# Performance work log

Measured on AMD Instinct MI355X. Metric: run time of the kernel, lower is better.

Reference implementation:

```python
import jax, jax.numpy as jnp
import numpy as np

EPS = 1e-5
HALT_THRESHOLD = 0.01
DILATIONS = (1, 2, 4)


def layer_norm(x, g, b):
    m = jnp.mean(x, axis=-1, keepdims=True)
    v = jnp.var(x, axis=-1, keepdims=True)
    return (x - m) * jax.lax.rsqrt(v + EPS) * g + b


def depthwise_conv(x, k, dilation):
    # x: [B,H,W,C], k: [kh,kw,1,C] (groups == C)
    pad = dilation * (k.shape[0] // 2)
    return jax.lax.conv_general_dilated(
        x, k, window_strides=(1, 1), padding=[(pad, pad), (pad, pad)],
        rhs_dilation=(dilation, dilation),
        dimension_numbers=('NHWC', 'HWIO', 'NHWC'),
        feature_group_count=x.shape[-1])


def setup_inputs() -> dict:
    key = jax.random.key(0)
    ks = jax.random.split(key, 12)
    B, H, W, C = 8, 96, 96, 64
    hid = 64
    P = C + len(DILATIONS) * C  # 256
    n = jax.random.normal
    return {
        'x': n(ks[0], (B, H, W, C), dtype=jnp.float32),
        'g1': jnp.ones((C,), jnp.float32), 'b1': jnp.zeros((C,), jnp.float32),
        'g2': jnp.ones((P,), jnp.float32), 'b2': jnp.zeros((P,), jnp.float32),
        'k1': 0.2 * n(ks[1], (3, 3, 1, C), dtype=jnp.float32),
        'k2': 0.2 * n(ks[2], (3, 3, 1, C), dtype=jnp.float32),
        'k3': 0.2 * n(ks[3], (3, 3, 1, C), dtype=jnp.float32),
        'Wu1': n(ks[4], (P, 2 * hid), dtype=jnp.float32) / np.sqrt(P),
        'bu1': jnp.zeros((2 * hid,), jnp.float32),
        'Wu2': n(ks[5], (2 * hid, hid), dtype=jnp.float32) / np.sqrt(2 * hid),
        'bu2': jnp.zeros((hid,), jnp.float32),
        'Wu3': n(ks[6], (hid, C), dtype=jnp.float32) / np.sqrt(hid),
        'bu3': jnp.zeros((C,), jnp.float32),
        'gh': jnp.ones((C,), jnp.float32), 'bh': jnp.zeros((C,), jnp.float32),
        'Wh1': n(ks[7], (C, hid), dtype=jnp.float32) / np.sqrt(C),
        'bh1': jnp.zeros((hid,), jnp.float32),
        'Wh2': n(ks[8], (hid, 1), dtype=jnp.float32) / np.sqrt(hid),
        'bh2': jnp.zeros((1,), jnp.float32),
        'max_steps': 8, 'min_steps': 1,
    }


def reference(x, g1, b1, g2, b2, k1, k2, k3, Wu1, bu1, Wu2, bu2, Wu3, bu3,
              gh, bh, Wh1, bh1, Wh2, bh2, max_steps, min_steps):
    gelu = lambda t: jax.nn.gelu(t, approximate=False)

    def forward_step(xs):
        # halt unit: LN -> Linear -> GELU -> Linear -> sigmoid
        h = gelu(layer_norm(xs, gh, bh) @ Wh1 + bh1)
        halt_probs = jax.nn.sigmoid(h @ Wh2 + bh2)[..., 0]  # [B,H,W]
        xn = layer_norm(xs, g1, b1)
        ps = [depthwise_conv(xn, k, d) for k, d in zip((k1, k2, k3), DILATIONS)]
        u = layer_norm(jnp.concatenate([xn] + ps, axis=-1), g2, b2)
        h1 = gelu(u @ Wu1 + bu1)
        h2 = gelu(h1 @ Wu2 + bu2)
        delta = h2 @ Wu3 + bu3
        return delta, halt_probs

    B, H, W, C = x.shape
    halted0 = jnp.zeros((B, H, W), jnp.bool_)
    acc0 = jnp.zeros((B, H, W), x.dtype)
    so0 = jnp.zeros_like(x)
    pc0 = jnp.zeros((B, H, W), x.dtype)

    def body(carry, step):
        xs, halted, acc, so, pc = carry
        delta, hp = forward_step(xs)
        active = ~halted
        af = active.astype(xs.dtype)
        xs = xs + delta * af[..., None]
        in_halt_phase = step >= (min_steps - 1)
        acc_n = acc + hp * af
        should_halt = (acc_n > 1.0 - HALT_THRESHOLD) & active
        halt_w = jnp.where(should_halt, 1.0 - (acc_n - hp), hp * af)
        so_n = so + xs * halt_w[..., None]
        halted_n = halted | should_halt
        acc = jnp.where(in_halt_phase, acc_n, acc)
        so = jnp.where(in_halt_phase, so_n, so)
        halted = jnp.where(in_halt_phase, halted_n, halted)
        pc = pc + jnp.where(in_halt_phase, af, jnp.ones_like(pc))
        return (xs, halted, acc, so, pc), None

    (xf, halted, acc, so, pc), _ = jax.lax.scan(
        body, (x, halted0, acc0, so0, pc0), jnp.arange(max_steps))
    # distribute remaining probability mass to cells that never halted
    remaining_w = (~halted).astype(x.dtype) * (1.0 - acc)
    so = so + xf * remaining_w[..., None]
    pc = pc / max_steps
    return so, halted, pc
```

## Files before the change

kernel.cpp:

```cpp
#include <hip/hip_runtime.h>
#include <hip/hip_bf16.h>

#define NPIX 73728
#define CH 64
#define HH 96
#define WW 96
#define PP 256

typedef __attribute__((ext_vector_type(8))) short short8;
typedef __attribute__((ext_vector_type(4))) float f32x4;

__device__ __forceinline__ float wsum64(float v) {
#pragma unroll
  for (int off = 32; off > 0; off >>= 1) v += __shfl_xor(v, off, 64);
  return v;
}
__device__ __forceinline__ float wsum16(float v) {
#pragma unroll
  for (int off = 1; off < 16; off <<= 1) v += __shfl_xor(v, off, 64);
  return v;
}
__device__ __forceinline__ float gelu_f(float x) {
  return 0.5f * x * (1.0f + erff(x * 0.70710678118654752f));
}
__device__ __forceinline__ float b2f(ushort u) {
  union { unsigned int i; float f; } c;
  c.i = ((unsigned int)u) << 16;
  return c.f;
}
__device__ __forceinline__ ushort f2b(float f) {
  union { float f; unsigned int i; } c;
  c.f = f;
  unsigned int r = c.i + 0x7fff + ((c.i >> 16) & 1);
  return (ushort)(r >> 16);
}

__global__ __launch_bounds__(256) void k_init(const float* __restrict__ x,
                                              float* __restrict__ xs,
                                              float* __restrict__ out,
                                              float* __restrict__ accb,
                                              float* __restrict__ xnf) {
  int i = blockIdx.x * 256 + threadIdx.x;
  if (i < NPIX * CH) xs[i] = x[i];
  if (i < NPIX * 66) out[i] = 0.0f;
  if (i < NPIX) { accb[i] = 0.0f; xnf[i] = 0.0f; }
}

__global__ __launch_bounds__(256) void k_wprep(const float* __restrict__ W,
                                               ushort* __restrict__ Wp, int K,
                                               int N) {
  int t = blockIdx.x * 256 + threadIdx.x;
  if (t >= K * N) return;
  int j = t & 7, l = (t >> 3) & 63, tile = t >> 9;
  int NT = N >> 4;
  int kt = tile / NT, nt = tile - kt * NT;
  int k = kt * 32 + ((l >> 4) & 3) * 8 + j;
  int n = nt * 16 + (l & 15);
  Wp[t] = f2b(W[k * N + n]);
}

__global__ __launch_bounds__(256) void k_ln_halt(
    const float* __restrict__ xs, ushort* __restrict__ xn, float* __restrict__ hp,
    const float* __restrict__ halted, float* __restrict__ xnf,
    const float* __restrict__ g1, const float* __restrict__ b1,
    const float* __restrict__ gh, const float* __restrict__ bh,
    const float* __restrict__ Wh1, const float* __restrict__ bh1,
    const float* __restrict__ Wh2, const float* __restrict__ bh2) {
  __shared__ float lnbuf[4][64];
  int wave = threadIdx.x >> 6, lane = threadIdx.x & 63;
  int pix = blockIdx.x * 4 + wave;
  float hf = halted[pix];
  if (hf != 0.0f && xnf[pix] != 0.0f) return;
  float x = xs[(size_t)pix * CH + lane];
  float mean = wsum64(x) * (1.0f / 64.0f);
  float d = x - mean;
  float var = wsum64(d * d) * (1.0f / 64.0f);
  float rstd = rsqrtf(var + 1e-5f);
  float nrm = d * rstd;
  xn[(size_t)pix * CH + lane] = f2b(nrm * g1[lane] + b1[lane]);
  lnbuf[wave][lane] = nrm * gh[lane] + bh[lane];
  float acc = bh1[lane];
#pragma unroll 8
  for (int i = 0; i < 64; ++i)
    acc = fmaf(lnbuf[wave][i], Wh1[i * 64 + lane], acc);
  acc = gelu_f(acc);
  float c = wsum64(acc * Wh2[lane]);
  if (lane == 0) {
    hp[pix] = 1.0f / (1.0f + expf(-(c + bh2[0])));
    xnf[pix] = hf;
  }
}

template <bool EDGE>
__device__ __forceinline__ void do_taps(const ushort* pb,
                                        const float* __restrict__ k1,
                                        const float* __restrict__ k2,
                                        const float* __restrict__ k3, int cg,
                                        int y, int xq, float (&br)[4][4]) {
#pragma unroll
  for (int t = 0; t < 3; ++t) {
    const int dl = (t == 0) ? 1 : ((t == 1) ? 2 : 4);
    const float* kk = (t == 0) ? k1 : ((t == 1) ? k2 : k3);
    float a0 = 0.f, a1 = 0.f, a2 = 0.f, a3 = 0.f;
#pragma unroll
    for (int ky = 0; ky < 3; ++ky) {
#pragma unroll
      for (int kx = 0; kx < 3; ++kx) {
        const int dy = (ky - 1) * dl, dx = (kx - 1) * dl;
        if (EDGE && !(ky == 1 && kx == 1)) {
          if ((unsigned)(y + dy) >= HH) continue;
        }
        const float4 w = *(const float4*)&kk[(ky * 3 + kx) * CH + cg * 4];
        float v0, v1, v2, v3;
        if (ky == 1 && kx == 1) {
          v0 = br[0][0]; v1 = br[0][1]; v2 = br[0][2]; v3 = br[0][3];
        } else {
          ushort4 d4 = *(const ushort4*)(pb + (dy * WW + dx) * CH);
          v0 = b2f(d4.x); v1 = b2f(d4.y); v2 = b2f(d4.z); v3 = b2f(d4.w);
          if (EDGE && (unsigned)(xq + dx) >= WW) {
            v0 = 0.f; v1 = 0.f; v2 = 0.f; v3 = 0.f;
          }
        }
        a0 = fmaf(v0, w.x, a0); a1 = fmaf(v1, w.y, a1);
        a2 = fmaf(v2, w.z, a2); a3 = fmaf(v3, w.w, a3);
      }
    }
    br[t + 1][0] = a0; br[t + 1][1] = a1;
    br[t + 1][2] = a2; br[t + 1][3] = a3;
  }
}

__global__ __launch_bounds__(256) void k_conv_u(
    const ushort* __restrict__ xn, ushort* __restrict__ u,
    const float* __restrict__ halted,
    const float* __restrict__ k1, const float* __restrict__ k2,
    const float* __restrict__ k3, const float* __restrict__ g2,
    const float* __restrict__ b2) {
  int wv = threadIdx.x >> 6, l = threadIdx.x & 63;
  int pix0 = blockIdx.x * 16 + wv * 4;
  int px = l >> 4, cg = l & 15;
  int pix = pix0 + px;
  if (__all(halted[pix] != 0.0f)) return;
  int b = pix0 / (HH * WW);
  int rem = pix0 - b * (HH * WW);
  int y = rem / WW, x0 = rem - (rem / WW) * WW;
  int xq = x0 + px;
  const ushort* pb = xn + (size_t)pix * CH + cg * 4;

  float br[4][4];
  {
    ushort4 c4 = *(const ushort4*)pb;
    br[0][0] = b2f(c4.x); br[0][1] = b2f(c4.y);
    br[0][2] = b2f(c4.z); br[0][3] = b2f(c4.w);
  }
  bool interior = (x0 >= 4) && (x0 <= WW - 8) && (y >= 4) && (y <= HH - 5);
  if (interior)
    do_taps<false>(pb, k1, k2, k3, cg, y, xq, br);
  else
    do_taps<true>(pb, k1, k2, k3, cg, y, xq, br);

  float s = 0.f;
#pragma unroll
  for (int t = 0; t < 4; ++t)
#pragma unroll
    for (int c = 0; c < 4; ++c) s += br[t][c];
  float mean = wsum16(s) * (1.0f / 256.0f);
  float vs = 0.f;
#pragma unroll
  for (int t = 0; t < 4; ++t)
#pragma unroll
    for (int c = 0; c < 4; ++c) {
      float d = br[t][c] - mean;
      vs += d * d;
    }
  float rstd = rsqrtf(wsum16(vs) * (1.0f / 256.0f) + 1e-5f);
  ushort* ub = u + (size_t)blockIdx.x * 4096;
  int lr16 = pix & 15;
#pragma unroll
  for (int t = 0; t < 4; ++t) {
    float4 g = *(const float4*)&g2[t * CH + cg * 4];
    float4 bb = *(const float4*)&b2[t * CH + cg * 4];
    ushort4 o;
    o.x = f2b((br[t][0] - mean) * rstd * g.x + bb.x);
    o.y = f2b((br[t][1] - mean) * rstd * g.y + bb.y);
    o.z = f2b((br[t][2] - mean) * rstd * g.z + bb.z);
    o.w = f2b((br[t][3] - mean) * rstd * g.w + bb.w);
    int k0 = t * 64 + cg * 4;
    int kt = k0 >> 5, lg = (k0 >> 3) & 3, jj = k0 & 7;
    *(ushort4*)(ub + kt * 512 + (lg * 16 + lr16) * 8 + jj) = o;
  }
}

__global__ __launch_bounds__(256) void k_mlp(
    const ushort* __restrict__ u, const ushort* __restrict__ Wp1,
    const ushort* __restrict__ Wp2, const ushort* __restrict__ Wp3,
    const float* __restrict__ bu1, const float* __restrict__ bu2,
    const float* __restrict__ bu3, const float* __restrict__ hp,
    float* __restrict__ xs, float* __restrict__ so, float* __restrict__ halted,
    float* __restrict__ accb, float* __restrict__ pc,
    const int* __restrict__ min_steps, int step) {
  __shared__ ushort h1s[4][16 * 136];
  __shared__ ushort h2s[4][16 * 72];
  int tid = threadIdx.x;
  int wv = tid >> 6, l = tid & 63;
  int p0 = blockIdx.x * 64 + wv * 16;
  int lr = l & 15, lg = l >> 4;
  if (__all(halted[p0 + lr] != 0.0f)) return;
  const f32x4 vzero = {0.0f, 0.0f, 0.0f, 0.0f};

  f32x4 acc1[8];
#pragma unroll
  for (int nt = 0; nt < 8; ++nt) acc1[nt] = vzero;
  const ushort* ub = u + (size_t)(blockIdx.x * 4 + wv) * 4096 + l * 8;
#pragma unroll
  for (int kt = 0; kt < 8; ++kt) {
    short8 a = *(const short8*)(ub + kt * 512);
#pragma unroll
    for (int nt = 0; nt < 8; ++nt) {
      short8 b = *(const short8*)(Wp1 + ((kt * 8 + nt) * 64 + l) * 8);
      acc1[nt] = __builtin_amdgcn_mfma_f32_16x16x32_bf16(a, b, acc1[nt], 0, 0, 0);
    }
  }
  ushort* h1w = h1s[wv];
#pragma unroll
  for (int nt = 0; nt < 8; ++nt) {
    float bb = bu1[nt * 16 + lr];
#pragma unroll
    for (int i = 0; i < 4; ++i)
      h1w[(lg * 4 + i) * 136 + nt * 16 + lr] = f2b(gelu_f(acc1[nt][i] + bb));
  }

  f32x4 acc2[4];
#pragma unroll
  for (int nt = 0; nt < 4; ++nt) acc2[nt] = vzero;
#pragma unroll
  for (int kt = 0; kt < 4; ++kt) {
    short8 a = *(const short8*)(h1w + lr * 136 + kt * 32 + lg * 8);
#pragma unroll
    for (int nt = 0; nt < 4; ++nt) {
      short8 b = *(const short8*)(Wp2 + ((kt * 4 + nt) * 64 + l) * 8);
      acc2[nt] = __builtin_amdgcn_mfma_f32_16x16x32_bf16(a, b, acc2[nt], 0, 0, 0);
    }
  }
  ushort* h2w = h2s[wv];
#pragma unroll
  for (int nt = 0; nt < 4; ++nt) {
    float bb = bu2[nt * 16 + lr];
#pragma unroll
    for (int i = 0; i < 4; ++i)
      h2w[(lg * 4 + i) * 72 + nt * 16 + lr] = f2b(gelu_f(acc2[nt][i] + bb));
  }

  f32x4 acc3[4];
#pragma unroll
  for (int nt = 0; nt < 4; ++nt) acc3[nt] = vzero;
#pragma unroll
  for (int kt = 0; kt < 2; ++kt) {
    short8 a = *(const short8*)(h2w + lr * 72 + kt * 32 + lg * 8);
#pragma unroll
    for (int nt = 0; nt < 4; ++nt) {
      short8 b = *(const short8*)(Wp3 + ((kt * 4 + nt) * 64 + l) * 8);
      acc3[nt] = __builtin_amdgcn_mfma_f32_16x16x32_bf16(a, b, acc3[nt], 0, 0, 0);
    }
  }
  float* df = (float*)h1w;
#pragma unroll
  for (int nt = 0; nt < 4; ++nt) {
    float bb = bu3[nt * 16 + lr];
#pragma unroll
    for (int i = 0; i < 4; ++i)
      df[(lg * 4 + i) * 68 + nt * 16 + lr] = acc3[nt][i] + bb;
  }

  int msteps = min_steps[0];
  bool in_halt = (step >= msteps - 1);
  int px = l >> 2, q = l & 3;
  int p = p0 + px;
  float hf = halted[p];
  float af = (hf == 0.0f) ? 1.0f : 0.0f;
  float hpv = hp[p];
  float accv = accb[p];
  float acc_n = accv + hpv * af;
  bool should_halt = (acc_n > 0.99f) && (af != 0.0f);
  float halt_w = should_halt ? (1.0f - (acc_n - hpv)) : hpv * af;
  size_t base = (size_t)p * CH + q * 16;
#pragma unroll
  for (int j = 0; j < 4; ++j) {
    float4 dv = *(const float4*)&df[px * 68 + q * 16 + j * 4];
    float4 xv = *(float4*)&xs[base + j * 4];
    xv.x += dv.x * af;
    xv.y += dv.y * af;
    xv.z += dv.z * af;
    xv.w += dv.w * af;
    *(float4*)&xs[base + j * 4] = xv;
    if (in_halt) {
      float4 sv = *(float4*)&so[base + j * 4];
      sv.x += xv.x * halt_w;
      sv.y += xv.y * halt_w;
      sv.z += xv.z * halt_w;
      sv.w += xv.w * halt_w;
      *(float4*)&so[base + j * 4] = sv;
    }
  }
  if (q == 0) {
    if (in_halt) {
      accb[p] = acc_n;
      halted[p] = (hf != 0.0f || should_halt) ? 1.0f : 0.0f;
    }
    pc[p] += in_halt ? af : 1.0f;
  }
}

__global__ __launch_bounds__(256) void k_final(
    const float* __restrict__ xs, float* __restrict__ so,
    const float* __restrict__ halted, const float* __restrict__ accb,
    float* __restrict__ pc, const int* __restrict__ max_steps) {
  int wave = threadIdx.x >> 6, lane = threadIdx.x & 63;
  int pix = blockIdx.x * 4 + wave;
  float rem = (halted[pix] == 0.0f) ? (1.0f - accb[pix]) : 0.0f;
  so[(size_t)pix * CH + lane] += xs[(size_t)pix * CH + lane] * rem;
  if (lane == 0) pc[pix] *= 1.0f / (float)max_steps[0];
}

extern "C" void kernel_launch(void* const* d_in, const int* in_sizes, int n_in,
                              void* d_out, int out_size, void* d_ws,
                              size_t ws_size, hipStream_t stream) {
  const float* x   = (const float*)d_in[0];
  const float* g1  = (const float*)d_in[1];
  const float* b1  = (const float*)d_in[2];
  const float* g2  = (const float*)d_in[3];
  const float* b2  = (const float*)d_in[4];
  const float* k1  = (const float*)d_in[5];
  const float* k2  = (const float*)d_in[6];
  const float* k3  = (const float*)d_in[7];
  const float* Wu1 = (const float*)d_in[8];
  const float* bu1 = (const float*)d_in[9];
  const float* Wu2 = (const float*)d_in[10];
  const float* bu2 = (const float*)d_in[11];
  const float* Wu3 = (const float*)d_in[12];
  const float* bu3 = (const float*)d_in[13];
  const float* gh  = (const float*)d_in[14];
  const float* bh  = (const float*)d_in[15];
  const float* Wh1 = (const float*)d_in[16];
  const float* bh1 = (const float*)d_in[17];
  const float* Wh2 = (const float*)d_in[18];
  const float* bh2 = (const float*)d_in[19];
  const int* max_steps = (const int*)d_in[20];
  const int* min_steps = (const int*)d_in[21];

  if (ws_size < (size_t)68000000) return;
  char* ws = (char*)d_ws;
  float*  xs   = (float*)(ws);
  ushort* xn   = (ushort*)(ws + 18874368);
  ushort* u    = (ushort*)(ws + 28311552);
  float*  hp   = (float*)(ws + 66060288);
  float*  accb = (float*)(ws + 66355200);
  ushort* Wp1  = (ushort*)(ws + 66650112);
  ushort* Wp2  = (ushort*)(ws + 66715648);
  ushort* Wp3  = (ushort*)(ws + 66732032);
  float*  xnf  = (float*)(ws + 66740224);
  float* so = (float*)d_out;
  float* halted = so + (size_t)NPIX * CH;
  float* pc = halted + NPIX;

  k_wprep<<<128, 256, 0, stream>>>(Wu1, Wp1, 256, 128);
  k_wprep<<<32, 256, 0, stream>>>(Wu2, Wp2, 128, 64);
  k_wprep<<<16, 256, 0, stream>>>(Wu3, Wp3, 64, 64);
  k_init<<<19008, 256, 0, stream>>>(x, xs, so, accb, xnf);
  for (int step = 0; step < 8; ++step) {
    k_ln_halt<<<NPIX / 4, 256, 0, stream>>>(xs, xn, hp, halted, xnf, g1, b1,
                                            gh, bh, Wh1, bh1, Wh2, bh2);
    k_conv_u<<<NPIX / 16, 256, 0, stream>>>(xn, u, halted, k1, k2, k3, g2, b2);
    k_mlp<<<NPIX / 64, 256, 0, stream>>>(u, Wp1, Wp2, Wp3, bu1, bu2, bu3, hp,
                                         xs, so, halted, accb, pc, min_steps,
                                         step);
  }
  k_final<<<NPIX / 4, 256, 0, stream>>>(xs, so, halted, accb, pc, max_steps);
}
```

Before: 735.8 us.

## Fuse dilated depthwise conv and LayerNorm into MLP kernel via LDS slab

Removes the separate conv+LN kernel that wrote the 256-channel bf16 activation tensor u to global memory. Each MLP wavefront now computes the conv taps and LayerNorm for its 16 pixels itself, writing directly into a per-wave LDS slab that the first MFMA GEMM reads from. The slab is then reused for the h1, h2 and delta scratch buffers. This saves a large global write and read plus one launch per step, at the cost of more LDS per block (32KB) and a longer, serial per-wave prologue before the MFMAs. The halt early-exit now also happens at 16-pixel wave granularity for the conv instead of 4.

```diff
diff --git a/kernel.cpp b/kernel.cpp
--- a/kernel.cpp
+++ b/kernel.cpp
@@ -130,98 +130,94 @@
   }
 }
 
-__global__ __launch_bounds__(256) void k_conv_u(
-    const ushort* __restrict__ xn, ushort* __restrict__ u,
-    const float* __restrict__ halted,
-    const float* __restrict__ k1, const float* __restrict__ k2,
-    const float* __restrict__ k3, const float* __restrict__ g2,
-    const float* __restrict__ b2) {
-  int wv = threadIdx.x >> 6, l = threadIdx.x & 63;
-  int pix0 = blockIdx.x * 16 + wv * 4;
-  int px = l >> 4, cg = l & 15;
-  int pix = pix0 + px;
-  if (__all(halted[pix] != 0.0f)) return;
-  int b = pix0 / (HH * WW);
-  int rem = pix0 - b * (HH * WW);
-  int y = rem / WW, x0 = rem - (rem / WW) * WW;
-  int xq = x0 + px;
-  const ushort* pb = xn + (size_t)pix * CH + cg * 4;
-
-  float br[4][4];
-  {
-    ushort4 c4 = *(const ushort4*)pb;
-    br[0][0] = b2f(c4.x); br[0][1] = b2f(c4.y);
-    br[0][2] = b2f(c4.z); br[0][3] = b2f(c4.w);
-  }
-  bool interior = (x0 >= 4) && (x0 <= WW - 8) && (y >= 4) && (y <= HH - 5);
-  if (interior)
-    do_taps<false>(pb, k1, k2, k3, cg, y, xq, br);
-  else
-    do_taps<true>(pb, k1, k2, k3, cg, y, xq, br);
-
-  float s = 0.f;
-#pragma unroll
-  for (int t = 0; t < 4; ++t)
-#pragma unroll
-    for (int c = 0; c < 4; ++c) s += br[t][c];
-  float mean = wsum16(s) * (1.0f / 256.0f);
-  float vs = 0.f;
-#pragma unroll
-  for (int t = 0; t < 4; ++t)
-#pragma unroll
-    for (int c = 0; c < 4; ++c) {
-      float d = br[t][c] - mean;
-      vs += d * d;
-    }
-  float rstd = rsqrtf(wsum16(vs) * (1.0f / 256.0f) + 1e-5f);
-  ushort* ub = u + (size_t)blockIdx.x * 4096;
-  int lr16 = pix & 15;
-#pragma unroll
-  for (int t = 0; t < 4; ++t) {
-    float4 g = *(const float4*)&g2[t * CH + cg * 4];
-    float4 bb = *(const float4*)&b2[t * CH + cg * 4];
-    ushort4 o;
-    o.x = f2b((br[t][0] - mean) * rstd * g.x + bb.x);
-    o.y = f2b((br[t][1] - mean) * rstd * g.y + bb.y);
-    o.z = f2b((br[t][2] - mean) * rstd * g.z + bb.z);
-    o.w = f2b((br[t][3] - mean) * rstd * g.w + bb.w);
-    int k0 = t * 64 + cg * 4;
-    int kt = k0 >> 5, lg = (k0 >> 3) & 3, jj = k0 & 7;
-    *(ushort4*)(ub + kt * 512 + (lg * 16 + lr16) * 8 + jj) = o;
-  }
-}
-
 __global__ __launch_bounds__(256) void k_mlp(
-    const ushort* __restrict__ u, const ushort* __restrict__ Wp1,
-    const ushort* __restrict__ Wp2, const ushort* __restrict__ Wp3,
-    const float* __restrict__ bu1, const float* __restrict__ bu2,
-    const float* __restrict__ bu3, const float* __restrict__ hp,
-    float* __restrict__ xs, float* __restrict__ so, float* __restrict__ halted,
+    const ushort* __restrict__ xn, const float* __restrict__ k1,
+    const float* __restrict__ k2, const float* __restrict__ k3,
+    const float* __restrict__ g2, const float* __restrict__ b2,
+    const ushort* __restrict__ Wp1, const ushort* __restrict__ Wp2,
+    const ushort* __restrict__ Wp3, const float* __restrict__ bu1,
+    const float* __restrict__ bu2, const float* __restrict__ bu3,
+    const float* __restrict__ hp, float* __restrict__ xs,
+    float* __restrict__ so, float* __restrict__ halted,
     float* __restrict__ accb, float* __restrict__ pc,
     const int* __restrict__ min_steps, int step) {
-  __shared__ ushort h1s[4][16 * 136];
-  __shared__ ushort h2s[4][16 * 72];
+  __shared__ ushort slab[4][4096];
   int tid = threadIdx.x;
   int wv = tid >> 6, l = tid & 63;
   int p0 = blockIdx.x * 64 + wv * 16;
   int lr = l & 15, lg = l >> 4;
   if (__all(halted[p0 + lr] != 0.0f)) return;
+  ushort* uw = slab[wv];
   const f32x4 vzero = {0.0f, 0.0f, 0.0f, 0.0f};
 
+  {
+    int cpx = l >> 4, cg = l & 15;
+#pragma unroll
+    for (int it = 0; it < 4; ++it) {
+      int pix0g = p0 + it * 4;
+      int b = pix0g / (HH * WW);
+      int rem = pix0g - b * (HH * WW);
+      int y = rem / WW, x0 = rem - (rem / WW) * WW;
+      int pix = pix0g + cpx;
+      int xq = x0 + cpx;
+      const ushort* pb = xn + (size_t)pix * CH + cg * 4;
+      float br[4][4];
+      {
+        ushort4 c4 = *(const ushort4*)pb;
+        br[0][0] = b2f(c4.x); br[0][1] = b2f(c4.y);
+        br[0][2] = b2f(c4.z); br[0][3] = b2f(c4.w);
+      }
+      bool interior = (x0 >= 4) && (x0 <= WW - 8) && (y >= 4) && (y <= HH - 5);
+      if (interior)
+        do_taps<false>(pb, k1, k2, k3, cg, y, xq, br);
+      else
+        do_taps<true>(pb, k1, k2, k3, cg, y, xq, br);
+
+      float s = 0.f;
+#pragma unroll
+      for (int t = 0; t < 4; ++t)
+#pragma unroll
+        for (int c = 0; c < 4; ++c) s += br[t][c];
+      float mean = wsum16(s) * (1.0f / 256.0f);
+      float vs = 0.f;
+#pragma unroll
+      for (int t = 0; t < 4; ++t)
+#pragma unroll
+        for (int c = 0; c < 4; ++c) {
+          float d = br[t][c] - mean;
+          vs += d * d;
+        }
+      float rstd = rsqrtf(wsum16(vs) * (1.0f / 256.0f) + 1e-5f);
+      int lr16 = it * 4 + cpx;
+#pragma unroll
+      for (int t = 0; t < 4; ++t) {
+        float4 g = *(const float4*)&g2[t * CH + cg * 4];
+        float4 bb = *(const float4*)&b2[t * CH + cg * 4];
+        ushort4 o;
+        o.x = f2b((br[t][0] - mean) * rstd * g.x + bb.x);
+        o.y = f2b((br[t][1] - mean) * rstd * g.y + bb.y);
+        o.z = f2b((br[t][2] - mean) * rstd * g.z + bb.z);
+        o.w = f2b((br[t][3] - mean) * rstd * g.w + bb.w);
+        int k0 = t * 64 + cg * 4;
+        int kt = k0 >> 5, lg2 = (k0 >> 3) & 3, jj = k0 & 7;
+        *(ushort4*)(uw + kt * 512 + (lg2 * 16 + lr16) * 8 + jj) = o;
+      }
+    }
+  }
+
   f32x4 acc1[8];
 #pragma unroll
   for (int nt = 0; nt < 8; ++nt) acc1[nt] = vzero;
-  const ushort* ub = u + (size_t)(blockIdx.x * 4 + wv) * 4096 + l * 8;
 #pragma unroll
   for (int kt = 0; kt < 8; ++kt) {
-    short8 a = *(const short8*)(ub + kt * 512);
+    short8 a = *(const short8*)(uw + kt * 512 + l * 8);
 #pragma unroll
     for (int nt = 0; nt < 8; ++nt) {
       short8 b = *(const short8*)(Wp1 + ((kt * 8 + nt) * 64 + l) * 8);
       acc1[nt] = __builtin_amdgcn_mfma_f32_16x16x32_bf16(a, b, acc1[nt], 0, 0, 0);
     }
   }
-  ushort* h1w = h1s[wv];
+  ushort* h1w = uw;
 #pragma unroll
   for (int nt = 0; nt < 8; ++nt) {
     float bb = bu1[nt * 16 + lr];
@@ -242,7 +238,7 @@
       acc2[nt] = __builtin_amdgcn_mfma_f32_16x16x32_bf16(a, b, acc2[nt], 0, 0, 0);
     }
   }
-  ushort* h2w = h2s[wv];
+  ushort* h2w = uw + 2176;
 #pragma unroll
   for (int nt = 0; nt < 4; ++nt) {
     float bb = bu2[nt * 16 + lr];
@@ -263,7 +259,7 @@
       acc3[nt] = __builtin_amdgcn_mfma_f32_16x16x32_bf16(a, b, acc3[nt], 0, 0, 0);
     }
   }
-  float* df = (float*)h1w;
+  float* df = (float*)uw;
 #pragma unroll
   for (int nt = 0; nt < 4; ++nt) {
     float bb = bu3[nt * 16 + lr];
@@ -348,17 +344,16 @@
   const int* max_steps = (const int*)d_in[20];
   const int* min_steps = (const int*)d_in[21];
 
-  if (ws_size < (size_t)68000000) return;
+  if (ws_size < (size_t)30000000) return;
   char* ws = (char*)d_ws;
   float*  xs   = (float*)(ws);
   ushort* xn   = (ushort*)(ws + 18874368);
-  ushort* u    = (ushort*)(ws + 28311552);
-  float*  hp   = (float*)(ws + 66060288);
-  float*  accb = (float*)(ws + 66355200);
-  ushort* Wp1  = (ushort*)(ws + 66650112);
-  ushort* Wp2  = (ushort*)(ws + 66715648);
-  ushort* Wp3  = (ushort*)(ws + 66732032);
-  float*  xnf  = (float*)(ws + 66740224);
+  float*  hp   = (float*)(ws + 28311552);
+  float*  accb = (float*)(ws + 28606464);
+  ushort* Wp1  = (ushort*)(ws + 28901376);
+  ushort* Wp2  = (ushort*)(ws + 28966912);
+  ushort* Wp3  = (ushort*)(ws + 28983296);
+  float*  xnf  = (float*)(ws + 28991488);
   float* so = (float*)d_out;
   float* halted = so + (size_t)NPIX * CH;
   float* pc = halted + NPIX;
@@ -370,10 +365,9 @@
   for (int step = 0; step < 8; ++step) {
     k_ln_halt<<<NPIX / 4, 256, 0, stream>>>(xs, xn, hp, halted, xnf, g1, b1,
                                             gh, bh, Wh1, bh1, Wh2, bh2);
-    k_conv_u<<<NPIX / 16, 256, 0, stream>>>(xn, u, halted, k1, k2, k3, g2, b2);
-    k_mlp<<<NPIX / 64, 256, 0, stream>>>(u, Wp1, Wp2, Wp3, bu1, bu2, bu3, hp,
-                                         xs, so, halted, accb, pc, min_steps,
-                                         step);
+    k_mlp<<<NPIX / 64, 256, 0, stream>>>(xn, k1, k2, k3, g2, b2, Wp1, Wp2, Wp3,
+                                         bu1, bu2, bu3, hp, xs, so, halted,
+                                         accb, pc, min_steps, step);
   }
   k_final<<<NPIX / 4, 256, 0, stream>>>(xs, so, halted, accb, pc, max_steps);
 }
```

New measurement: 824.3 us. 1.12x slower.
